# Performance work log

Hardware: AMD Instinct MI355X
Metric: run time of the kernel (lower is better)

## Reference

```python
import jax, jax.numpy as jnp
import numpy as np
from jax import lax

B, T, C = 64, 512, 512  # time_step == channel required by LayerNorm([T, C]) on [B, C, T]
T2 = T // 2  # downsampled length for scale 1 (conv kernel=2, stride=2)
LN_EPS = 1e-5


def _hardswish(x):
    return x * jnp.clip(x + 3.0, 0.0, 6.0) / 6.0


def _triu_mix(z, W, b):
    # TriU: out[..., i] = Linear_i(z[..., 0:i+1]) == causal lower-triangular mixing
    # z: [B, C, T'], W: [T', T'] (row i holds weights of linear i), b: [T']
    mask = jnp.tril(jnp.ones(W.shape, z.dtype))
    return jnp.einsum('bcj,ij->bci', z, W * mask) + b


def setup_inputs() -> dict:
    key = jax.random.key(0)
    ks = jax.random.split(key, 13)
    s = 0.02
    return {
        'x': jax.random.normal(ks[0], (B, T, C), jnp.float32),
        'ln_gamma': jnp.ones((T, C), jnp.float32),
        'ln_beta': jnp.zeros((T, C), jnp.float32),
        'w1': jax.random.normal(ks[1], (T, T), jnp.float32) * s,
        'b1': jax.random.normal(ks[2], (T,), jnp.float32) * s,
        'w2': jax.random.normal(ks[3], (T, T), jnp.float32) * s,
        'b2': jax.random.normal(ks[4], (T,), jnp.float32) * s,
        'conv_w': jax.random.normal(ks[5], (C, C, 2), jnp.float32) * s,  # OIH
        'conv_b': jax.random.normal(ks[6], (C,), jnp.float32) * s,
        'w3': jax.random.normal(ks[7], (T2, T2), jnp.float32) * s,
        'b3': jax.random.normal(ks[8], (T2,), jnp.float32) * s,
        'w4': jax.random.normal(ks[9], (T2, T2), jnp.float32) * s,
        'b4': jax.random.normal(ks[10], (T2,), jnp.float32) * s,
    }


def reference(x, ln_gamma, ln_beta, w1, b1, w2, b2, conv_w, conv_b, w3, b3, w4, b4):
    xp = jnp.transpose(x, (0, 2, 1))  # [B, C, T]
    # scale 0: LayerNorm over last two dims (C, T jointly), affine weight [T, C] == [C, T] positionally
    mean = jnp.mean(xp, axis=(-2, -1), keepdims=True)
    var = jnp.var(xp, axis=(-2, -1), keepdims=True)
    xn = (xp - mean) / jnp.sqrt(var + LN_EPS) * ln_gamma + ln_beta
    y = _triu_mix(xn, w1, b1)
    y = _hardswish(y)
    y = _triu_mix(y, w2, b2)
    # scale 1: Conv1d(C, C, kernel=2, stride=2) then TriU/Hardswish/TriU on length T/2
    z = lax.conv_general_dilated(xp, conv_w, window_strides=(2,), padding='VALID',
                                 dimension_numbers=('NCH', 'OIH', 'NCH'))
    z = z + conv_b[None, :, None]
    z = _triu_mix(z, w3, b3)
    z = _hardswish(z)
    z = _triu_mix(z, w4, b4)
    return jnp.concatenate([y, z], axis=-1)  # [B, C, T + T/2]
```

## Files before the change

### kernel.cpp

```cpp
#include <hip/hip_runtime.h>
#include <hip/hip_bf16.h>


#define NB 64

typedef __bf16 bf16x8 __attribute__((ext_vector_type(8)));
typedef __bf16 bf16x4 __attribute__((ext_vector_type(4)));
typedef float f32x4 __attribute__((ext_vector_type(4)));

#define AS_GLOBAL __attribute__((address_space(1)))
#define AS_LDS    __attribute__((address_space(3)))

__global__ void pre1_k(const float* __restrict__ x, float* __restrict__ part,
                       __bf16* __restrict__ xbf, const float* __restrict__ cw,
                       __bf16* __restrict__ WtT) {
  if (blockIdx.x < 256) {
    int bb = blockIdx.x;
    int b = bb >> 2, q = bb & 3;
    size_t base = (size_t)b * 262144 + (size_t)q * 65536;
    const float4* xb = (const float4*)(x + base);
    bf16x4* xo = (bf16x4*)(xbf + base);
    float s = 0.f, ss = 0.f;
    for (int it = 0; it < 64; ++it) {
      int idx = threadIdx.x + 256 * it;
      float4 v = xb[idx];
      s += (v.x + v.y) + (v.z + v.w);
      ss += (v.x * v.x + v.y * v.y) + (v.z * v.z + v.w * v.w);
      bf16x4 o;
      o[0] = (__bf16)v.x; o[1] = (__bf16)v.y; o[2] = (__bf16)v.z; o[3] = (__bf16)v.w;
      xo[idx] = o;
    }
    __shared__ float ls[256], lss[256];
    ls[threadIdx.x] = s; lss[threadIdx.x] = ss;
    __syncthreads();
    for (int off = 128; off > 0; off >>= 1) {
      if (threadIdx.x < off) {
        ls[threadIdx.x] += ls[threadIdx.x + off];
        lss[threadIdx.x] += lss[threadIdx.x + off];
      }
      __syncthreads();
    }
    if (threadIdx.x == 0) { part[bb * 2] = ls[0]; part[bb * 2 + 1] = lss[0]; }
    return;
  }
  int idx = (blockIdx.x - 256) * 256 + threadIdx.x;
  int o = idx >> 10, r = idx & 1023;
  int i = r & 511, k = r >> 9;
  WtT[idx] = (__bf16)cw[(size_t)o * 1024 + i * 2 + k];
}

template <bool MASKK, bool HSW, bool ROWB, bool COLB, bool OUTBF>
__device__ __forceinline__ void gemm_body(
    int bid, int lgx, __bf16* As, __bf16* Bs,
    const __bf16* __restrict__ A, long sAb,
    const __bf16* __restrict__ Bt, long sBb,
    void* __restrict__ Cm, long sCb,
    const float* __restrict__ bias,
    int K, int ldc, int c_off) {
  const int tid = threadIdx.x;
  const int lane = tid & 63, wid = tid >> 6;
  const int wm = (wid >> 1) * 64, wn = (wid & 1) * 64;
  const int lr = lane & 15, lg = lane >> 4;

  const int nid = ((bid & 7) << (lgx + 5)) | (bid >> 3);
  const int bm = (nid & ((1 << lgx) - 1)) * 128;
  const int bn = ((nid >> lgx) & 3) * 128;
  const int bz = nid >> (lgx + 2);

  const int srg = lane >> 3;
  const int ssrc = ((lane & 7) ^ srg) << 3;

  const __bf16* gA[4];
  const __bf16* gB[4];
#pragma unroll
  for (int p = 0; p < 4; ++p) {
    int row = p * 32 + wid * 8 + srg;
    gA[p] = A + (size_t)bz * sAb + (size_t)(bm + row) * K + ssrc;
    gB[p] = Bt + (size_t)bz * sBb + (size_t)(bn + row) * K + ssrc;
  }

  f32x4 acc[4][4] = {};

  const int Kend = MASKK ? (bm + 128) : K;
  for (int k0 = 0; k0 < Kend; k0 += 64) {
#pragma unroll
    for (int p = 0; p < 4; ++p) {
      __builtin_amdgcn_global_load_lds(
          (const AS_GLOBAL void*)gA[p],
          (AS_LDS void*)&As[(p * 32 + wid * 8) * 64], 16, 0, 0);
      __builtin_amdgcn_global_load_lds(
          (const AS_GLOBAL void*)gB[p],
          (AS_LDS void*)&Bs[(p * 32 + wid * 8) * 64], 16, 0, 0);
      gA[p] += 64;
      gB[p] += 64;
    }
    __syncthreads();
#pragma unroll
    for (int kk = 0; kk < 64; kk += 32) {
      bf16x8 af[4], bfv[4];
#pragma unroll
      for (int f = 0; f < 4; ++f) {
        int ar = wm + f * 16 + lr;
        af[f] = *(const bf16x8*)&As[ar * 64 + ((kk + lg * 8) ^ ((ar & 7) << 3))];
        int br = wn + f * 16 + lr;
        bfv[f] = *(const bf16x8*)&Bs[br * 64 + ((kk + lg * 8) ^ ((br & 7) << 3))];
      }
#pragma unroll
      for (int i = 0; i < 4; ++i)
#pragma unroll
        for (int j = 0; j < 4; ++j)
          acc[i][j] = __builtin_amdgcn_mfma_f32_16x16x32_bf16(af[i], bfv[j], acc[i][j], 0, 0, 0);
    }
    __syncthreads();
  }

#pragma unroll
  for (int i = 0; i < 4; ++i) {
    int row0 = bm + wm + i * 16 + lg * 4;
    float rb0 = 0.f, rb1 = 0.f, rb2 = 0.f, rb3 = 0.f;
    if (ROWB) { rb0 = bias[row0]; rb1 = bias[row0 + 1]; rb2 = bias[row0 + 2]; rb3 = bias[row0 + 3]; }
#pragma unroll
    for (int j = 0; j < 4; ++j) {
      int col = bn + wn + j * 16 + lr;
      float cbv = COLB ? bias[col] : 0.f;
      float v[4] = {acc[i][j][0] + rb0 + cbv, acc[i][j][1] + rb1 + cbv,
                    acc[i][j][2] + rb2 + cbv, acc[i][j][3] + rb3 + cbv};
      if (HSW) {
#pragma unroll
        for (int r = 0; r < 4; ++r) {
          float u = fminf(fmaxf(v[r] + 3.f, 0.f), 6.f);
          v[r] = v[r] * u * (1.f / 6.f);
        }
      }
      if (OUTBF) {
        __bf16* C = (__bf16*)Cm + (size_t)bz * sCb;
        bf16x4 o;
        o[0] = (__bf16)v[0]; o[1] = (__bf16)v[1]; o[2] = (__bf16)v[2]; o[3] = (__bf16)v[3];
        *(bf16x4*)&C[(size_t)col * ldc + c_off + row0] = o;
      } else {
        float* C = (float*)Cm + (size_t)bz * sCb;
        *(float4*)&C[(size_t)col * ldc + c_off + row0] =
            make_float4(v[0], v[1], v[2], v[3]);
      }
    }
  }
}

__device__ __forceinline__ void norm_body(
    int bid, char* smem,
    const __bf16* __restrict__ xbf, const float* __restrict__ g,
    const float* __restrict__ be, const float* __restrict__ part,
    __bf16* __restrict__ XnT) {
  float (*ls)[65] = (float(*)[65])smem;
  int b = bid >> 6;
  int r = bid & 63;
  int bc = (r & 7) * 64;
  int bt = (r >> 3) * 64;
  int tid = threadIdx.x;
  float s = 0.f, ss = 0.f;
#pragma unroll
  for (int q = 0; q < 4; ++q) { s += part[(b * 4 + q) * 2]; ss += part[(b * 4 + q) * 2 + 1]; }
  float mean = s * (1.f / 262144.f);
  float istd = rsqrtf(ss * (1.f / 262144.f) - mean * mean + 1e-5f);

  const __bf16* xb = xbf + (size_t)b * 262144;
  int row = tid >> 3;
  int ch = (tid & 7) * 8;
#pragma unroll
  for (int p = 0; p < 2; ++p) {
    int t = p * 32 + row;
    bf16x8 v = *(const bf16x8*)&xb[(size_t)(bt + t) * 512 + bc + ch];
#pragma unroll
    for (int j = 0; j < 8; ++j) ls[t][ch + j] = (float)v[j];
  }
  __syncthreads();
  int cr = tid >> 3;
  int t0 = (tid & 7) * 8;
  __bf16* xnb = XnT + (size_t)b * 262144;
#pragma unroll
  for (int p = 0; p < 2; ++p) {
    int cg = bc + p * 32 + cr;
    int cl = p * 32 + cr;
    float4 g0 = *(const float4*)&g[(size_t)cg * 512 + bt + t0];
    float4 g1 = *(const float4*)&g[(size_t)cg * 512 + bt + t0 + 4];
    float4 e0 = *(const float4*)&be[(size_t)cg * 512 + bt + t0];
    float4 e1 = *(const float4*)&be[(size_t)cg * 512 + bt + t0 + 4];
    float gv[8] = {g0.x, g0.y, g0.z, g0.w, g1.x, g1.y, g1.z, g1.w};
    float ev[8] = {e0.x, e0.y, e0.z, e0.w, e1.x, e1.y, e1.z, e1.w};
    bf16x8 o;
#pragma unroll
    for (int j = 0; j < 8; ++j) {
      float xh = (ls[t0 + j][cl] - mean) * istd;
      o[j] = (__bf16)(xh * gv[j] + ev[j]);
    }
    *(bf16x8*)&xnb[(size_t)cg * 512 + bt + t0] = o;
  }
}

__global__ __launch_bounds__(256, 3) void fused_g3_norm_k(
    const __bf16* __restrict__ xbf, const __bf16* __restrict__ WtT,
    __bf16* __restrict__ Z1T, const float* __restrict__ cb,
    const float* __restrict__ g, const float* __restrict__ be,
    const float* __restrict__ part, __bf16* __restrict__ XnT,
    const float* __restrict__ w1, const float* __restrict__ w2,
    const float* __restrict__ w3, const float* __restrict__ w4,
    __bf16* __restrict__ w1b, __bf16* __restrict__ w2b,
    __bf16* __restrict__ w3b, __bf16* __restrict__ w4b) {
  __shared__ __align__(16) char smem[33280];
  __bf16* As = (__bf16*)smem;
  __bf16* Bs = (__bf16*)(smem + 16384);
  int bid = blockIdx.x;
  if (bid < 512) {
    gemm_body<false, false, false, true, true>(bid, 1, As, Bs,
        xbf, 262144, WtT, 0, Z1T, 131072, cb, 1024, 256, 0);
  } else if (bid < 4608) {
    norm_body(bid - 512, smem, xbf, g, be, part, XnT);
  } else {
    int idx = (bid - 4608) * 256 + threadIdx.x;
    if (idx < 262144) { int i = idx >> 9, j = idx & 511; w1b[idx] = (__bf16)(j <= i ? w1[idx] : 0.f); return; }
    idx -= 262144;
    if (idx < 262144) { int i = idx >> 9, j = idx & 511; w2b[idx] = (__bf16)(j <= i ? w2[idx] : 0.f); return; }
    idx -= 262144;
    if (idx < 65536) { int i = idx >> 8, j = idx & 255; w3b[idx] = (__bf16)(j <= i ? w3[idx] : 0.f); return; }
    idx -= 65536;
    { int i = idx >> 8, j = idx & 255; w4b[idx] = (__bf16)(j <= i ? w4[idx] : 0.f); }
  }
}

__global__ __launch_bounds__(256, 3) void fused_g1_g4_k(
    const __bf16* __restrict__ w1b, const __bf16* __restrict__ XnT,
    __bf16* __restrict__ Y1T, const float* __restrict__ b1,
    const __bf16* __restrict__ w3b, const __bf16* __restrict__ Z1T,
    __bf16* __restrict__ Z3T, const float* __restrict__ b3) {
  __shared__ __align__(16) char smem[32768];
  __bf16* As = (__bf16*)smem;
  __bf16* Bs = (__bf16*)(smem + 16384);
  int bid = blockIdx.x;
  if (bid < 1024)
    gemm_body<true, true, true, false, true>(bid, 2, As, Bs,
        w1b, 0, XnT, 262144, Y1T, 262144, b1, 512, 512, 0);
  else
    gemm_body<true, true, true, false, true>(bid - 1024, 1, As, Bs,
        w3b, 0, Z1T, 131072, Z3T, 131072, b3, 256, 256, 0);
}

__global__ __launch_bounds__(256, 3) void fused_g2_g5_k(
    const __bf16* __restrict__ w2b, const __bf16* __restrict__ Y1T,
    float* __restrict__ out, const float* __restrict__ b2,
    const __bf16* __restrict__ w4b, const __bf16* __restrict__ Z3T,
    const float* __restrict__ b4) {
  __shared__ __align__(16) char smem[32768];
  __bf16* As = (__bf16*)smem;
  __bf16* Bs = (__bf16*)(smem + 16384);
  int bid = blockIdx.x;
  if (bid < 1024)
    gemm_body<true, false, true, false, false>(bid, 2, As, Bs,
        w2b, 0, Y1T, 262144, out, 393216, b2, 512, 768, 0);
  else
    gemm_body<true, false, true, false, false>(bid - 1024, 1, As, Bs,
        w4b, 0, Z3T, 131072, out, 393216, b4, 256, 768, 512);
}

extern "C" void kernel_launch(void* const* d_in, const int* in_sizes, int n_in,
                              void* d_out, int out_size, void* d_ws, size_t ws_size,
                              hipStream_t stream) {
  const float* x  = (const float*)d_in[0];
  const float* g  = (const float*)d_in[1];
  const float* be = (const float*)d_in[2];
  const float* w1 = (const float*)d_in[3];
  const float* b1 = (const float*)d_in[4];
  const float* w2 = (const float*)d_in[5];
  const float* b2 = (const float*)d_in[6];
  const float* cw = (const float*)d_in[7];
  const float* cb = (const float*)d_in[8];
  const float* w3 = (const float*)d_in[9];
  const float* b3 = (const float*)d_in[10];
  const float* w4 = (const float*)d_in[11];
  const float* b4 = (const float*)d_in[12];
  float* out = (float*)d_out;

  char* ws = (char*)d_ws;
  float*  part  = (float*)(ws + 4096);
  __bf16* w1b   = (__bf16*)(ws + (1 << 20));
  __bf16* w2b   = (__bf16*)(ws + (1 << 20) + 524288);
  __bf16* w3b   = (__bf16*)(ws + (2 << 20));
  __bf16* w4b   = (__bf16*)(ws + (2 << 20) + 131072);
  __bf16* WtT   = (__bf16*)(ws + (3 << 20));
  __bf16* xbf   = (__bf16*)(ws + ((size_t)4 << 20));
  __bf16* XnT   = (__bf16*)(ws + ((size_t)36 << 20));
  __bf16* Y1T   = (__bf16*)(ws + ((size_t)68 << 20));
  __bf16* Z1T   = (__bf16*)(ws + ((size_t)100 << 20));
  __bf16* Z3T   = (__bf16*)(ws + ((size_t)116 << 20));

  pre1_k<<<2304, 256, 0, stream>>>(x, part, xbf, cw, WtT);
  fused_g3_norm_k<<<7168, 256, 0, stream>>>(xbf, WtT, Z1T, cb, g, be, part, XnT,
                                            w1, w2, w3, w4, w1b, w2b, w3b, w4b);
  fused_g1_g4_k<<<1536, 256, 0, stream>>>(w1b, XnT, Y1T, b1, w3b, Z1T, Z3T, b3);
  fused_g2_g5_k<<<1536, 256, 0, stream>>>(w2b, Y1T, out, b2, w4b, Z3T, b4);
}
```

Baseline: 128.9 us.

## Merge four kernels into one persistent cooperative kernel with grid syncs

Replaces the four separate launches (stats/cast, conv GEMM+norm+weight prep, first TriU GEMMs, second TriU GEMMs) with one persistent cooperative kernel. The grid is sized from occupancy and capped at 768 blocks; each block loops over the virtual block IDs of each phase, with grid-wide syncs between phases. The aim is to remove launch gaps and per-kernel tail drain. In exchange there are grid-barrier costs, a fixed, possibly lower block count for the large phases, extra __syncthreads for shared-memory reuse, and a per-call occupancy query on the host.

```diff
diff --git a/kernel.cpp b/kernel.cpp
--- a/kernel.cpp
+++ b/kernel.cpp
@@ -1,5 +1,8 @@
 #include <hip/hip_runtime.h>
 #include <hip/hip_bf16.h>
+#include <hip/hip_cooperative_groups.h>
+
+namespace cg = cooperative_groups;
 
 
 #define NB 64
@@ -11,12 +14,13 @@
 #define AS_GLOBAL __attribute__((address_space(1)))
 #define AS_LDS    __attribute__((address_space(3)))
 
-__global__ void pre1_k(const float* __restrict__ x, float* __restrict__ part,
-                       __bf16* __restrict__ xbf, const float* __restrict__ cw,
-                       __bf16* __restrict__ WtT) {
-  if (blockIdx.x < 256) {
-    int bb = blockIdx.x;
-    int b = bb >> 2, q = bb & 3;
+__device__ __forceinline__ void pre1_body(
+    int vb, char* smem,
+    const float* __restrict__ x, float* __restrict__ part,
+    __bf16* __restrict__ xbf, const float* __restrict__ cw,
+    __bf16* __restrict__ WtT) {
+  if (vb < 256) {
+    int b = vb >> 2, q = vb & 3;
     size_t base = (size_t)b * 262144 + (size_t)q * 65536;
     const float4* xb = (const float4*)(x + base);
     bf16x4* xo = (bf16x4*)(xbf + base);
@@ -30,7 +34,8 @@
       o[0] = (__bf16)v.x; o[1] = (__bf16)v.y; o[2] = (__bf16)v.z; o[3] = (__bf16)v.w;
       xo[idx] = o;
     }
-    __shared__ float ls[256], lss[256];
+    float* ls = (float*)smem;
+    float* lss = ls + 256;
     ls[threadIdx.x] = s; lss[threadIdx.x] = ss;
     __syncthreads();
     for (int off = 128; off > 0; off >>= 1) {
@@ -40,13 +45,29 @@
       }
       __syncthreads();
     }
-    if (threadIdx.x == 0) { part[bb * 2] = ls[0]; part[bb * 2 + 1] = lss[0]; }
+    if (threadIdx.x == 0) { part[vb * 2] = ls[0]; part[vb * 2 + 1] = lss[0]; }
+    __syncthreads();
     return;
   }
-  int idx = (blockIdx.x - 256) * 256 + threadIdx.x;
+  int idx = (vb - 256) * 256 + threadIdx.x;
   int o = idx >> 10, r = idx & 1023;
   int i = r & 511, k = r >> 9;
   WtT[idx] = (__bf16)cw[(size_t)o * 1024 + i * 2 + k];
+}
+
+__device__ __forceinline__ void wprep_body(
+    int vb, const float* __restrict__ w1, const float* __restrict__ w2,
+    const float* __restrict__ w3, const float* __restrict__ w4,
+    __bf16* __restrict__ w1b, __bf16* __restrict__ w2b,
+    __bf16* __restrict__ w3b, __bf16* __restrict__ w4b) {
+  int idx = vb * 256 + threadIdx.x;
+  if (idx < 262144) { int i = idx >> 9, j = idx & 511; w1b[idx] = (__bf16)(j <= i ? w1[idx] : 0.f); return; }
+  idx -= 262144;
+  if (idx < 262144) { int i = idx >> 9, j = idx & 511; w2b[idx] = (__bf16)(j <= i ? w2[idx] : 0.f); return; }
+  idx -= 262144;
+  if (idx < 65536) { int i = idx >> 8, j = idx & 255; w3b[idx] = (__bf16)(j <= i ? w3[idx] : 0.f); return; }
+  idx -= 65536;
+  { int i = idx >> 8, j = idx & 255; w4b[idx] = (__bf16)(j <= i ? w4[idx] : 0.f); }
 }
 
 template <bool MASKK, bool HSW, bool ROWB, bool COLB, bool OUTBF>
@@ -166,6 +187,7 @@
   const __bf16* xb = xbf + (size_t)b * 262144;
   int row = tid >> 3;
   int ch = (tid & 7) * 8;
+  __syncthreads();
 #pragma unroll
   for (int p = 0; p < 2; ++p) {
     int t = p * 32 + row;
@@ -197,68 +219,59 @@
   }
 }
 
-__global__ __launch_bounds__(256, 3) void fused_g3_norm_k(
-    const __bf16* __restrict__ xbf, const __bf16* __restrict__ WtT,
-    __bf16* __restrict__ Z1T, const float* __restrict__ cb,
-    const float* __restrict__ g, const float* __restrict__ be,
-    const float* __restrict__ part, __bf16* __restrict__ XnT,
+__global__ __launch_bounds__(256, 3) void mega_k(
+    const float* __restrict__ x, const float* __restrict__ g,
+    const float* __restrict__ be, const float* __restrict__ cw,
     const float* __restrict__ w1, const float* __restrict__ w2,
     const float* __restrict__ w3, const float* __restrict__ w4,
-    __bf16* __restrict__ w1b, __bf16* __restrict__ w2b,
-    __bf16* __restrict__ w3b, __bf16* __restrict__ w4b) {
+    const float* __restrict__ b1, const float* __restrict__ b2,
+    const float* __restrict__ b3, const float* __restrict__ b4,
+    const float* __restrict__ cb, float* __restrict__ out,
+    float* __restrict__ part, __bf16* __restrict__ xbf,
+    __bf16* __restrict__ WtT, __bf16* __restrict__ XnT,
+    __bf16* __restrict__ Y1T, __bf16* __restrict__ Z1T,
+    __bf16* __restrict__ Z3T, __bf16* __restrict__ w1b,
+    __bf16* __restrict__ w2b, __bf16* __restrict__ w3b,
+    __bf16* __restrict__ w4b) {
+  cg::grid_group gg = cg::this_grid();
   __shared__ __align__(16) char smem[33280];
   __bf16* As = (__bf16*)smem;
   __bf16* Bs = (__bf16*)(smem + 16384);
-  int bid = blockIdx.x;
-  if (bid < 512) {
-    gemm_body<false, false, false, true, true>(bid, 1, As, Bs,
-        xbf, 262144, WtT, 0, Z1T, 131072, cb, 1024, 256, 0);
-  } else if (bid < 4608) {
-    norm_body(bid - 512, smem, xbf, g, be, part, XnT);
-  } else {
-    int idx = (bid - 4608) * 256 + threadIdx.x;
-    if (idx < 262144) { int i = idx >> 9, j = idx & 511; w1b[idx] = (__bf16)(j <= i ? w1[idx] : 0.f); return; }
-    idx -= 262144;
-    if (idx < 262144) { int i = idx >> 9, j = idx & 511; w2b[idx] = (__bf16)(j <= i ? w2[idx] : 0.f); return; }
-    idx -= 262144;
-    if (idx < 65536) { int i = idx >> 8, j = idx & 255; w3b[idx] = (__bf16)(j <= i ? w3[idx] : 0.f); return; }
-    idx -= 65536;
-    { int i = idx >> 8, j = idx & 255; w4b[idx] = (__bf16)(j <= i ? w4[idx] : 0.f); }
-  }
-}
-
-__global__ __launch_bounds__(256, 3) void fused_g1_g4_k(
-    const __bf16* __restrict__ w1b, const __bf16* __restrict__ XnT,
-    __bf16* __restrict__ Y1T, const float* __restrict__ b1,
-    const __bf16* __restrict__ w3b, const __bf16* __restrict__ Z1T,
-    __bf16* __restrict__ Z3T, const float* __restrict__ b3) {
-  __shared__ __align__(16) char smem[32768];
-  __bf16* As = (__bf16*)smem;
-  __bf16* Bs = (__bf16*)(smem + 16384);
-  int bid = blockIdx.x;
-  if (bid < 1024)
-    gemm_body<true, true, true, false, true>(bid, 2, As, Bs,
-        w1b, 0, XnT, 262144, Y1T, 262144, b1, 512, 512, 0);
-  else
-    gemm_body<true, true, true, false, true>(bid - 1024, 1, As, Bs,
-        w3b, 0, Z1T, 131072, Z3T, 131072, b3, 256, 256, 0);
-}
-
-__global__ __launch_bounds__(256, 3) void fused_g2_g5_k(
-    const __bf16* __restrict__ w2b, const __bf16* __restrict__ Y1T,
-    float* __restrict__ out, const float* __restrict__ b2,
-    const __bf16* __restrict__ w4b, const __bf16* __restrict__ Z3T,
-    const float* __restrict__ b4) {
-  __shared__ __align__(16) char smem[32768];
-  __bf16* As = (__bf16*)smem;
-  __bf16* Bs = (__bf16*)(smem + 16384);
-  int bid = blockIdx.x;
-  if (bid < 1024)
-    gemm_body<true, false, true, false, false>(bid, 2, As, Bs,
-        w2b, 0, Y1T, 262144, out, 393216, b2, 512, 768, 0);
-  else
-    gemm_body<true, false, true, false, false>(bid - 1024, 1, As, Bs,
-        w4b, 0, Z3T, 131072, out, 393216, b4, 256, 768, 512);
+  const int G = gridDim.x;
+
+  for (int vb = blockIdx.x; vb < 2304; vb += G)
+    pre1_body(vb, smem, x, part, xbf, cw, WtT);
+  gg.sync();
+
+  for (int vb = blockIdx.x; vb < 7168; vb += G) {
+    if (vb < 512)
+      gemm_body<false, false, false, true, true>(vb, 1, As, Bs,
+          xbf, 262144, WtT, 0, Z1T, 131072, cb, 1024, 256, 0);
+    else if (vb < 4608)
+      norm_body(vb - 512, smem, xbf, g, be, part, XnT);
+    else
+      wprep_body(vb - 4608, w1, w2, w3, w4, w1b, w2b, w3b, w4b);
+  }
+  gg.sync();
+
+  for (int vb = blockIdx.x; vb < 1536; vb += G) {
+    if (vb < 1024)
+      gemm_body<true, true, true, false, true>(vb, 2, As, Bs,
+          w1b, 0, XnT, 262144, Y1T, 262144, b1, 512, 512, 0);
+    else
+      gemm_body<true, true, true, false, true>(vb - 1024, 1, As, Bs,
+          w3b, 0, Z1T, 131072, Z3T, 131072, b3, 256, 256, 0);
+  }
+  gg.sync();
+
+  for (int vb = blockIdx.x; vb < 1536; vb += G) {
+    if (vb < 1024)
+      gemm_body<true, false, true, false, false>(vb, 2, As, Bs,
+          w2b, 0, Y1T, 262144, out, 393216, b2, 512, 768, 0);
+    else
+      gemm_body<true, false, true, false, false>(vb - 1024, 1, As, Bs,
+          w4b, 0, Z3T, 131072, out, 393216, b4, 256, 768, 512);
+  }
 }
 
 extern "C" void kernel_launch(void* const* d_in, const int* in_sizes, int n_in,
@@ -292,9 +305,21 @@
   __bf16* Z1T   = (__bf16*)(ws + ((size_t)100 << 20));
   __bf16* Z3T   = (__bf16*)(ws + ((size_t)116 << 20));
 
-  pre1_k<<<2304, 256, 0, stream>>>(x, part, xbf, cw, WtT);
-  fused_g3_norm_k<<<7168, 256, 0, stream>>>(xbf, WtT, Z1T, cb, g, be, part, XnT,
-                                            w1, w2, w3, w4, w1b, w2b, w3b, w4b);
-  fused_g1_g4_k<<<1536, 256, 0, stream>>>(w1b, XnT, Y1T, b1, w3b, Z1T, Z3T, b3);
-  fused_g2_g5_k<<<1536, 256, 0, stream>>>(w2b, Y1T, out, b2, w4b, Z3T, b4);
-}
+  int nb = 0;
+  hipOccupancyMaxActiveBlocksPerMultiprocessor(&nb, mega_k, 256, 0);
+  if (nb < 1) nb = 1;
+  long grid = (long)nb * 256;
+  if (grid > 768) grid = 768;
+  grid &= ~7L;
+  if (grid < 8) grid = 8;
+
+  void* args[] = {
+      (void*)&x, (void*)&g, (void*)&be, (void*)&cw,
+      (void*)&w1, (void*)&w2, (void*)&w3, (void*)&w4,
+      (void*)&b1, (void*)&b2, (void*)&b3, (void*)&b4,
+      (void*)&cb, (void*)&out,
+      (void*)&part, (void*)&xbf, (void*)&WtT, (void*)&XnT,
+      (void*)&Y1T, (void*)&Z1T, (void*)&Z3T,
+      (void*)&w1b, (void*)&w2b, (void*)&w3b, (void*)&w4b};
+  hipLaunchCooperativeKernel(mega_k, dim3((int)grid), dim3(256), args, 0, stream);
+}
```

Measured after the change: 316.5 us. 2.46x slower.
